# Performance work log

Measured on AMD Instinct MI355X. Metric: run time of the kernel, lower is better.

The kernel has to match this reference:

```python
import jax, jax.numpy as jnp
import numpy as np

BIN_NUM = 256
HIDDEN = 1024
B, S = 128, 1024
FEAT = BIN_NUM - 1          # 255
LAST = FEAT + 3             # 258, used as d_k in the original code


def setup_inputs() -> dict:
    key = jax.random.key(0)
    ks = jax.random.split(key, 8)

    def lin(k, out_d, in_d):
        # kaiming_uniform_ with relu nonlinearity: bound = sqrt(6/in_d)
        bound = np.sqrt(6.0 / in_d)
        return jax.random.uniform(k, (out_d, in_d), jnp.float32, -bound, bound)

    return {
        "input_tensor": jax.random.normal(ks[0], (B, S, LAST), jnp.float32),
        "kW": lin(ks[1], HIDDEN, FEAT), "kb": jnp.zeros((HIDDEN,), jnp.float32),
        "vW": lin(ks[2], HIDDEN, FEAT), "vb": jnp.zeros((HIDDEN,), jnp.float32),
        "qW": lin(ks[3], HIDDEN, 3),    "qb": jnp.zeros((HIDDEN,), jnp.float32),
        "W1": lin(ks[4], HIDDEN // 2, HIDDEN),      "b1": jnp.zeros((HIDDEN // 2,), jnp.float32),
        "W2": lin(ks[5], HIDDEN // 4, HIDDEN // 2), "b2": jnp.zeros((HIDDEN // 4,), jnp.float32),
        "W3": lin(ks[6], 2, HIDDEN // 4),           "b3": jnp.zeros((2,), jnp.float32),
    }


def reference(input_tensor, kW, kb, vW, vb, qW, qb, W1, b1, W2, b2, W3, b3):
    d_k = input_tensor.shape[-1]                      # NOTE: full last dim (258)
    feats = input_tensor[..., :FEAT]                  # [B,S,255]
    archi = input_tensor[:, 0, FEAT:][:, None, :]     # [B,1,3]

    k = jnp.einsum('bsf,hf->bsh', feats, kW) + kb     # [B,S,H]
    v = jnp.einsum('bsf,hf->bsh', feats, vW) + vb     # [B,S,H]
    q = jnp.einsum('bqf,hf->bqh', archi, qW) + qb     # [B,1,H]

    scores = jnp.einsum('bqh,bsh->bqs', q, k) / jnp.sqrt(jnp.float32(d_k))
    attn = jax.nn.softmax(scores, axis=-1)            # [B,1,S]
    res = jnp.einsum('bqs,bsh->bqh', attn, v)[:, 0, :]  # squeeze -> [B,H]

    # classifier (dropout is identity at inference)
    h = jax.nn.relu(res @ W1.T + b1)
    h = jax.nn.relu(h @ W2.T + b2)
    return h @ W3.T + b3                              # [B,2]
```

## Files before the change

kernel.cpp:

```cpp
#include <hip/hip_runtime.h>
#include <stdint.h>

#define NBATCH 128
#define SEQ    1024
#define ROWE   258
#define NPART  16

#define WS_KQP   0
#define WS_PART  524288
#define WS_WF    2654208
#define WS_REST  2785280
#define WS_H1P   3309568


static __device__ __forceinline__ float fexp2(float x){ return __builtin_amdgcn_exp2f(x); }

__global__ __launch_bounds__(256) void qk_kernel(const float* __restrict__ in,
    const float* __restrict__ kW, const float* __restrict__ qW,
    const float* __restrict__ qb, float* __restrict__ kqp,
    float* __restrict__ h1pre, float* __restrict__ out)
{
    __shared__ float qv[2][256];
    const int bb = blockIdx.x;
    const int hh = blockIdx.y;
    const int t  = threadIdx.x;
    const int b0 = bb * 2;
    if (hh == 0) {
        h1pre[(size_t)b0 * 512 + t]             = 0.f;
        h1pre[(size_t)b0 * 512 + 256 + t]       = 0.f;
        h1pre[(size_t)(b0 + 1) * 512 + t]       = 0.f;
        h1pre[(size_t)(b0 + 1) * 512 + 256 + t] = 0.f;
        if (t < 4) out[b0 * 2 + t] = 0.f;
    }
    const int h = hh * 256 + t;
    const float w0 = qW[h * 3 + 0], w1 = qW[h * 3 + 1], w2 = qW[h * 3 + 2], bq = qb[h];
    #pragma unroll
    for (int u = 0; u < 2; u++) {
        const size_t abase = (size_t)(b0 + u) * (SEQ * ROWE) + 255;
        qv[u][t] = bq + in[abase] * w0 + in[abase + 1] * w1 + in[abase + 2] * w2;
    }
    __syncthreads();
    const int col = (t < 255) ? t : 254;
    const float* kWp = kW + (size_t)(hh * 256) * 255 + col;
    float acc0 = 0.f, acc1 = 0.f;
    #pragma unroll 16
    for (int i = 0; i < 256; i++) {
        const float kv = kWp[(size_t)i * 255];
        acc0 = fmaf(qv[0][i], kv, acc0);
        acc1 = fmaf(qv[1][i], kv, acc1);
    }
    kqp[(size_t)((hh << 7) + b0) * 256 + t]       = (t < 255) ? acc0 : 0.f;
    kqp[(size_t)((hh << 7) + b0 + 1) * 256 + t]   = (t < 255) ? acc1 : 0.f;
}

__global__ __launch_bounds__(256, 4) void attn_kernel(const float* __restrict__ in,
                                                      const float* __restrict__ kqp,
                                                      float* __restrict__ part)
{
    __shared__ float sM[8], sL[8], sacc[8][256];
    const int p = blockIdx.x, b = blockIdx.y;
    const int t = threadIdx.x, w = t >> 6, lane = t & 63;
    const int hf = lane >> 5, sub = lane & 31;

    const float SCALE = (float)(1.4426950408889634 / 16.062378404209142);
    float k[8];
    {
        float s0x=0.f,s0y=0.f,s0z=0.f,s0w=0.f, s1x=0.f,s1y=0.f,s1z=0.f,s1w=0.f;
        #pragma unroll
        for (int hh = 0; hh < 4; hh++) {
            const float4* pp = (const float4*)(kqp + (size_t)((hh << 7) + b) * 256 + sub * 8);
            const float4 u = pp[0], v = pp[1];
            s0x+=u.x; s0y+=u.y; s0z+=u.z; s0w+=u.w;
            s1x+=v.x; s1y+=v.y; s1z+=v.z; s1w+=v.w;
        }
        k[0]=s0x*SCALE; k[1]=s0y*SCALE; k[2]=s0z*SCALE; k[3]=s0w*SCALE;
        k[4]=s1x*SCALE; k[5]=s1y*SCALE; k[6]=s1z*SCALE; k[7]=s1w*SCALE;
    }

    const float* rp = in + ((size_t)b * SEQ + p * 64 + w * 16 + hf) * ROWE + sub * 8;

    float x[8], xn[8], a[8];
    #pragma unroll
    for (int j = 0; j < 8; j++) a[j] = 0.f;
    #pragma unroll
    for (int j = 0; j < 8; j += 2) {
        const float2 v2 = *(const float2*)(rp + j);
        x[j] = v2.x; x[j+1] = v2.y;
    }
    rp += 2 * ROWE;
    float m = -INFINITY, l = 0.f;

    #pragma unroll
    for (int i = 0; i < 8; i++) {
        if (i < 7) {
            #pragma unroll
            for (int j = 0; j < 8; j += 2) {
                const float2 v2 = *(const float2*)(rp + j);
                xn[j] = v2.x; xn[j+1] = v2.y;
            }
            rp += 2 * ROWE;
        }
        const float d0 = fmaf(x[0], k[0], x[1] * k[1]);
        const float d1 = fmaf(x[2], k[2], x[3] * k[3]);
        const float d2 = fmaf(x[4], k[4], x[5] * k[5]);
        const float d3 = fmaf(x[6], k[6], x[7] * k[7]);
        float d = (d0 + d1) + (d2 + d3);
        #pragma unroll
        for (int off = 16; off > 0; off >>= 1) d += __shfl_xor(d, off, 64);
        const float mn = fmaxf(m, d);
        const float cc = fexp2(m - mn);
        const float wt = fexp2(d - mn);
        l = fmaf(l, cc, wt);
        #pragma unroll
        for (int j = 0; j < 8; j++) a[j] = fmaf(a[j], cc, wt * x[j]);
        m = mn;
        if (i < 7) {
            #pragma unroll
            for (int j = 0; j < 8; j++) x[j] = xn[j];
        }
    }

    const int id = w * 2 + hf;
    #pragma unroll
    for (int j = 0; j < 8; j += 2)
        *(float2*)(&sacc[id][sub * 8 + j]) = make_float2(a[j], a[j+1]);
    if (sub == 0) { sM[id] = m; sL[id] = l; }
    __syncthreads();

    float M = sM[0];
    #pragma unroll
    for (int q = 1; q < 8; q++) M = fmaxf(M, sM[q]);
    float c[8];
    #pragma unroll
    for (int q = 0; q < 8; q++) c[q] = fexp2(sM[q] - M);
    float acc = 0.f, Lm = 0.f;
    #pragma unroll
    for (int q = 0; q < 8; q++) { acc = fmaf(c[q], sacc[q][t], acc); Lm = fmaf(c[q], sL[q], Lm); }
    float* o = part + ((size_t)b * NPART + p) * 260;
    o[t] = acc;
    if (t == 0) { o[256] = M; o[257] = Lm; }
}

__global__ __launch_bounds__(256) void comb_kernel(const float* __restrict__ part,
                                                   float* __restrict__ wf)
{
    const int b = blockIdx.x, t = threadIdx.x;
    const float* pb = part + (size_t)b * NPART * 260;
    float M = -INFINITY;
    #pragma unroll
    for (int p = 0; p < NPART; p++) M = fmaxf(M, pb[p * 260 + 256]);
    float L = 0.f, acc = 0.f;
    #pragma unroll
    for (int p = 0; p < NPART; p++) {
        const float cc = fexp2(pb[p * 260 + 256] - M);
        L   = fmaf(cc, pb[p * 260 + 257], L);
        acc = fmaf(cc, pb[p * 260 + t], acc);
    }
    wf[b * 256 + t] = (t < 255) ? acc / L : 0.f;
}

__global__ __launch_bounds__(512) void res_kernel(const float* __restrict__ vW,
                                                  const float* __restrict__ vb,
                                                  const float* __restrict__ wf,
                                                  float* __restrict__ resT)
{
    __shared__ float vws[8][256];
    __shared__ float wfs[64][130];
    const int g = blockIdx.x, t = threadIdx.x;
    #pragma unroll
    for (int i = 0; i < 4; i++) {
        const int idx = i * 512 + t, f = idx & 255, hh = idx >> 8;
        vws[hh][f] = (f < 255) ? vW[(g * 8 + hh) * 255 + f] : 0.f;
    }
    const int b = t & 127, ho = t >> 7;
    const int fl = t & 63, wv = t >> 6;
    float acc0 = 0.f, acc1 = 0.f;
    for (int c = 0; c < 4; c++) {
        __syncthreads();
        #pragma unroll
        for (int i = 0; i < 16; i++) {
            const int bb = i * 8 + wv;
            wfs[fl][bb] = wf[bb * 256 + c * 64 + fl];
        }
        __syncthreads();
        #pragma unroll 8
        for (int f = 0; f < 64; f++) {
            const float w2 = wfs[f][b];
            acc0 = fmaf(w2, vws[ho][c * 64 + f], acc0);
            acc1 = fmaf(w2, vws[ho + 4][c * 64 + f], acc1);
        }
    }
    const int h0 = g * 8 + ho, h1 = h0 + 4;
    resT[h0 * 128 + b] = acc0 + vb[h0];
    resT[h1 * 128 + b] = acc1 + vb[h1];
}

__global__ __launch_bounds__(256) void h1_kernel(const float* __restrict__ W1,
                                                 const float* __restrict__ resT,
                                                 float* __restrict__ h1pre)
{
    __shared__ float W1s[16][256];
    __shared__ float ress[64][66];
    const int j0 = blockIdx.x * 16, b0 = blockIdx.y * 64, h0 = blockIdx.z * 256;
    const int t = threadIdx.x;
    #pragma unroll
    for (int i = 0; i < 16; i++) {
        const int idx = i * 256 + t, hl = idx & 255, jj = idx >> 8;
        W1s[jj][hl] = W1[(j0 + jj) * 1024 + h0 + hl];
    }
    const int bb = t & 63, jg = t >> 6;
    float acc[4] = {0.f, 0.f, 0.f, 0.f};
    for (int sc = 0; sc < 4; sc++) {
        __syncthreads();
        {
            const int bl = t & 63, wvv = t >> 6;
            #pragma unroll
            for (int i = 0; i < 16; i++) {
                const int hl = i * 4 + wvv;
                ress[hl][bl] = resT[(h0 + sc * 64 + hl) * 128 + b0 + bl];
            }
        }
        __syncthreads();
        #pragma unroll 4
        for (int hl = 0; hl < 64; hl++) {
            const float rv = ress[hl][bb];
            acc[0] = fmaf(rv, W1s[jg * 4 + 0][sc * 64 + hl], acc[0]);
            acc[1] = fmaf(rv, W1s[jg * 4 + 1][sc * 64 + hl], acc[1]);
            acc[2] = fmaf(rv, W1s[jg * 4 + 2][sc * 64 + hl], acc[2]);
            acc[3] = fmaf(rv, W1s[jg * 4 + 3][sc * 64 + hl], acc[3]);
        }
    }
    #pragma unroll
    for (int k = 0; k < 4; k++)
        atomicAdd(&h1pre[(size_t)(b0 + bb) * 512 + j0 + jg * 4 + k], acc[k]);
}

__global__ __launch_bounds__(256) void h2out_kernel(const float* __restrict__ W2,
    const float* __restrict__ b1, const float* __restrict__ b2,
    const float* __restrict__ W3, const float* __restrict__ b3,
    const float* __restrict__ h1pre, float* __restrict__ out)
{
    __shared__ float W2s[8][512];
    __shared__ float h1s[64][66];
    __shared__ float po[4][64][2];
    const int j20 = blockIdx.x * 8, b0 = blockIdx.y * 64;
    const int t = threadIdx.x;
    #pragma unroll
    for (int i = 0; i < 16; i++) {
        const int idx = i * 256 + t, jl = idx & 511, jj = idx >> 9;
        W2s[jj][jl] = W2[(j20 + jj) * 512 + jl];
    }
    const int bb = t & 63, jg = t >> 6;
    float acc[2] = {0.f, 0.f};
    for (int sc = 0; sc < 8; sc++) {
        __syncthreads();
        {
            const int jl = t & 63, wvv = t >> 6;
            #pragma unroll
            for (int i = 0; i < 16; i++) {
                const int bl = i * 4 + wvv;
                const float v = h1pre[(size_t)(b0 + bl) * 512 + sc * 64 + jl] + b1[sc * 64 + jl];
                h1s[jl][bl] = fmaxf(v, 0.f);
            }
        }
        __syncthreads();
        #pragma unroll 4
        for (int jl = 0; jl < 64; jl++) {
            const float hv = h1s[jl][bb];
            acc[0] = fmaf(hv, W2s[jg * 2 + 0][sc * 64 + jl], acc[0]);
            acc[1] = fmaf(hv, W2s[jg * 2 + 1][sc * 64 + jl], acc[1]);
        }
    }
    float p0 = 0.f, p1 = 0.f;
    #pragma unroll
    for (int k = 0; k < 2; k++) {
        const int j2 = j20 + jg * 2 + k;
        const float h2v = fmaxf(acc[k] + b2[j2], 0.f);
        p0 = fmaf(h2v, W3[j2],       p0);
        p1 = fmaf(h2v, W3[256 + j2], p1);
    }
    po[jg][bb][0] = p0;
    po[jg][bb][1] = p1;
    __syncthreads();
    if (t < 128) {
        const int b = t & 63, o = t >> 6;
        float s = po[0][b][o] + po[1][b][o] + po[2][b][o] + po[3][b][o];
        if (blockIdx.x == 0) s += b3[o];
        atomicAdd(&out[(b0 + b) * 2 + o], s);
    }
}

extern "C" void kernel_launch(void* const* d_in, const int* in_sizes, int n_in,
                              void* d_out, int out_size, void* d_ws, size_t ws_size,
                              hipStream_t stream)
{
    (void)in_sizes; (void)n_in; (void)out_size; (void)ws_size;
    const float* in = (const float*)d_in[0];
    const float* kW = (const float*)d_in[1];
    const float* vW = (const float*)d_in[3];
    const float* vb = (const float*)d_in[4];
    const float* qW = (const float*)d_in[5];
    const float* qb = (const float*)d_in[6];
    const float* W1 = (const float*)d_in[7];
    const float* b1 = (const float*)d_in[8];
    const float* W2 = (const float*)d_in[9];
    const float* b2 = (const float*)d_in[10];
    const float* W3 = (const float*)d_in[11];
    const float* b3 = (const float*)d_in[12];

    char* ws = (char*)d_ws;
    float* kqp   = (float*)(ws + WS_KQP);
    float* part  = (float*)(ws + WS_PART);
    float* wf    = (float*)(ws + WS_WF);
    float* resT  = (float*)(ws + WS_REST);
    float* h1pre = (float*)(ws + WS_H1P);

    qk_kernel   <<<dim3(64, 4),         256, 0, stream>>>(in, kW, qW, qb, kqp, h1pre, (float*)d_out);
    attn_kernel <<<dim3(NPART, NBATCH), 256, 0, stream>>>(in, kqp, part);
    comb_kernel <<<128,                 256, 0, stream>>>(part, wf);
    res_kernel  <<<128,                 512, 0, stream>>>(vW, vb, wf, resT);
    h1_kernel   <<<dim3(32, 2, 4),      256, 0, stream>>>(W1, resT, h1pre);
    h2out_kernel<<<dim3(32, 2),         256, 0, stream>>>(W2, b1, b2, W3, b3, h1pre, (float*)d_out);
}
```

Baseline: 276.9 us.

## Halve sequence partitions and process two rows per step with deeper prefetch

Result: slower. 317.0 us (+14.5%).

```diff
diff --git a/kernel.cpp b/kernel.cpp
--- a/kernel.cpp
+++ b/kernel.cpp
@@ -4,7 +4,7 @@
 #define NBATCH 128
 #define SEQ    1024
 #define ROWE   258
-#define NPART  16
+#define NPART  8
 
 #define WS_KQP   0
 #define WS_PART  524288
@@ -77,46 +77,74 @@
         k[4]=s1x*SCALE; k[5]=s1y*SCALE; k[6]=s1z*SCALE; k[7]=s1w*SCALE;
     }
 
-    const float* rp = in + ((size_t)b * SEQ + p * 64 + w * 16 + hf) * ROWE + sub * 8;
-
-    float x[8], xn[8], a[8];
+    const float* rp = in + ((size_t)b * SEQ + p * 128 + w * 32 + hf) * ROWE + sub * 8;
+
+    float x0[8], x1[8], p0[8], p1[8], a[8];
     #pragma unroll
     for (int j = 0; j < 8; j++) a[j] = 0.f;
     #pragma unroll
     for (int j = 0; j < 8; j += 2) {
-        const float2 v2 = *(const float2*)(rp + j);
-        x[j] = v2.x; x[j+1] = v2.y;
-    }
-    rp += 2 * ROWE;
+        float2 v2;
+        v2 = *(const float2*)(rp + 0 * 2 * ROWE + j); x0[j] = v2.x; x0[j+1] = v2.y;
+        v2 = *(const float2*)(rp + 1 * 2 * ROWE + j); x1[j] = v2.x; x1[j+1] = v2.y;
+        v2 = *(const float2*)(rp + 2 * 2 * ROWE + j); p0[j] = v2.x; p0[j+1] = v2.y;
+        v2 = *(const float2*)(rp + 3 * 2 * ROWE + j); p1[j] = v2.x; p1[j+1] = v2.y;
+    }
     float m = -INFINITY, l = 0.f;
 
     #pragma unroll
-    for (int i = 0; i < 8; i++) {
-        if (i < 7) {
+    for (int it = 0; it < 8; it++) {
+        float n0[8], n1[8];
+        if (it < 6) {
+            const float* q4 = rp + (size_t)(2 * it + 4) * 2 * ROWE;
+            const float* q5 = rp + (size_t)(2 * it + 5) * 2 * ROWE;
             #pragma unroll
             for (int j = 0; j < 8; j += 2) {
-                const float2 v2 = *(const float2*)(rp + j);
-                xn[j] = v2.x; xn[j+1] = v2.y;
+                float2 v2;
+                v2 = *(const float2*)(q4 + j); n0[j] = v2.x; n0[j+1] = v2.y;
+                v2 = *(const float2*)(q5 + j); n1[j] = v2.x; n1[j+1] = v2.y;
             }
-            rp += 2 * ROWE;
-        }
-        const float d0 = fmaf(x[0], k[0], x[1] * k[1]);
-        const float d1 = fmaf(x[2], k[2], x[3] * k[3]);
-        const float d2 = fmaf(x[4], k[4], x[5] * k[5]);
-        const float d3 = fmaf(x[6], k[6], x[7] * k[7]);
-        float d = (d0 + d1) + (d2 + d3);
+        }
+        float d0, d1;
+        {
+            const float u0 = fmaf(x0[0], k[0], x0[1] * k[1]);
+            const float u1 = fmaf(x0[2], k[2], x0[3] * k[3]);
+            const float u2 = fmaf(x0[4], k[4], x0[5] * k[5]);
+            const float u3 = fmaf(x0[6], k[6], x0[7] * k[7]);
+            d0 = (u0 + u1) + (u2 + u3);
+            const float v0 = fmaf(x1[0], k[0], x1[1] * k[1]);
+            const float v1 = fmaf(x1[2], k[2], x1[3] * k[3]);
+            const float v2 = fmaf(x1[4], k[4], x1[5] * k[5]);
+            const float v3 = fmaf(x1[6], k[6], x1[7] * k[7]);
+            d1 = (v0 + v1) + (v2 + v3);
+        }
         #pragma unroll
-        for (int off = 16; off > 0; off >>= 1) d += __shfl_xor(d, off, 64);
-        const float mn = fmaxf(m, d);
-        const float cc = fexp2(m - mn);
-        const float wt = fexp2(d - mn);
-        l = fmaf(l, cc, wt);
+        for (int off = 16; off > 0; off >>= 1) {
+            d0 += __shfl_xor(d0, off, 64);
+            d1 += __shfl_xor(d1, off, 64);
+        }
+        {
+            const float mn = fmaxf(m, d0);
+            const float cc = fexp2(m - mn);
+            const float wt = fexp2(d0 - mn);
+            l = fmaf(l, cc, wt);
+            #pragma unroll
+            for (int j = 0; j < 8; j++) a[j] = fmaf(a[j], cc, wt * x0[j]);
+            m = mn;
+        }
+        {
+            const float mn = fmaxf(m, d1);
+            const float cc = fexp2(m - mn);
+            const float wt = fexp2(d1 - mn);
+            l = fmaf(l, cc, wt);
+            #pragma unroll
+            for (int j = 0; j < 8; j++) a[j] = fmaf(a[j], cc, wt * x1[j]);
+            m = mn;
+        }
         #pragma unroll
-        for (int j = 0; j < 8; j++) a[j] = fmaf(a[j], cc, wt * x[j]);
-        m = mn;
-        if (i < 7) {
-            #pragma unroll
-            for (int j = 0; j < 8; j++) x[j] = xn[j];
+        for (int j = 0; j < 8; j++) {
+            x0[j] = p0[j]; x1[j] = p1[j];
+            if (it < 6) { p0[j] = n0[j]; p1[j] = n1[j]; }
         }
     }
 
```
